# Kernel tuning notes

Hardware: AMD Instinct MI355X
Metric: run time of the kernel (lower is better)

## Reference

```python
import jax, jax.numpy as jnp
import numpy as np
from jax import lax

TAU_MIN = 0.01
TAU_MAX = 10.0
SLOW_TAU = 5.0


def setup_inputs() -> dict:
    key = jax.random.key(0)
    ks = iter(jax.random.split(key, 40))
    def p(shape, scale=0.05):
        return (jax.random.normal(next(ks), shape, jnp.float32) * scale)
    B, T, D = 1024, 512, 31
    FU, SU, H = 32, 32, 64
    inp = {
        "x": jax.random.normal(next(ks), (B, T, D), jnp.float32),
        # FlashFloodGate: Linear(62->32), Linear(32->1)
        "fg_w1": p((32, 2 * D)), "fg_b1": p((32,)),
        "fg_w2": p((1, 32)), "fg_b2": p((1,)),
        # fast LTC cell
        "fwin": p((FU, D)), "fbin": p((FU,)), "fwrec": p((FU, FU)),
        # slow LTC cell
        "swin": p((SU, D)), "sbin": p((SU,)), "swrec": p((SU, SU)),
        # fusion Linear(64->64)
        "fu_w": p((H, FU + SU)), "fu_b": p((H,)),
        # attention Linear(64->32), Linear(32->1)
        "at_w1": p((32, H)), "at_b1": p((32,)),
        "at_w2": p((1, 32)), "at_b2": p((1,)),
        # depth head Linear(64->64), Linear(64->5)
        "d_w1": p((64, H)), "d_b1": p((64,)),
        "d_w2": p((5, 64)), "d_b2": p((5,)),
        # overflow head Linear(64->64), Linear(64->32), Linear(32->1)
        "o_w1": p((64, H)), "o_b1": p((64,)),
        "o_w2": p((32, 64)), "o_b2": p((32,)),
        "o_w3": p((1, 32)), "o_b3": p((1,)),
        # intensity head Linear(64->32), Linear(32->1)
        "i_w1": p((32, H)), "i_b1": p((32,)),
        "i_w2": p((1, 32)), "i_b2": p((1,)),
    }
    return inp


def _ltc_scan(pre_tbh, w_rec, tau_tb1, h0):
    # pre_tbh: [T,B,H] precomputed W_in x + b; tau_tb1 broadcastable to [T,B,1]
    def step(h, inp):
        pre_t, tau_t = inp
        upd = jnp.tanh(pre_t + h @ w_rec.T)
        h = h + (upd - h) / tau_t
        return h, h
    _, hs = lax.scan(step, h0, (pre_tbh, tau_tb1))
    return jnp.transpose(hs, (1, 0, 2))  # [B,T,H]


def _forward(x, fg_w1, fg_b1, fg_w2, fg_b2, fwin, fbin, fwrec, swin, sbin, swrec,
             fu_w, fu_b, at_w1, at_b1, at_w2, at_b2, d_w1, d_b1, d_w2, d_b2,
             o_w1, o_b1, o_w2, o_b2, o_w3, o_b3, i_w1, i_b1, i_w2, i_b2):
    B, T, D = x.shape
    # FlashFloodGate over all timesteps (x_prev of t=0 is x_0 -> dx=0)
    dx = jnp.concatenate([jnp.zeros_like(x[:, :1]), x[:, 1:] - x[:, :-1]], axis=1)
    ci = jnp.concatenate([x, dx], axis=-1)                       # [B,T,2D]
    cs = jax.nn.sigmoid(jnp.tanh(ci @ fg_w1.T + fg_b1) @ fg_w2.T + fg_b2)  # [B,T,1]
    tau_fast = TAU_MAX - cs * (TAU_MAX - TAU_MIN)                # [B,T,1]
    # fast LTC (stepwise tau)
    pre_f = jnp.transpose(x @ fwin.T + fbin, (1, 0, 2))          # [T,B,FU]
    fast = _ltc_scan(pre_f, fwrec, jnp.transpose(tau_fast, (1, 0, 2)),
                     jnp.zeros((B, fwrec.shape[0]), x.dtype))
    # slow LTC (constant tau = 5.0, shape [B,1])
    pre_s = jnp.transpose(x @ swin.T + sbin, (1, 0, 2))          # [T,B,SU]
    slow = _ltc_scan(pre_s, swrec, jnp.full((T, 1, 1), SLOW_TAU, x.dtype),
                     jnp.zeros((B, swrec.shape[0]), x.dtype))
    # fusion
    ltc = jnp.tanh(jnp.concatenate([fast, slow], axis=-1) @ fu_w.T + fu_b)  # [B,T,H]
    # attention over time
    logits = jnp.tanh(ltc @ at_w1.T + at_b1) @ at_w2.T + at_b2   # [B,T,1]
    attn = jax.nn.softmax(logits, axis=1)
    context = jnp.sum(ltc * attn, axis=1)                        # [B,H]
    # heads (dropout is identity in eval)
    depths = jax.nn.relu(context @ d_w1.T + d_b1) @ d_w2.T + d_b2
    overflow = jax.nn.sigmoid(
        jax.nn.relu(jax.nn.relu(context @ o_w1.T + o_b1) @ o_w2.T + o_b2) @ o_w3.T + o_b3)
    intensity = jax.nn.sigmoid(jax.nn.relu(context @ i_w1.T + i_b1) @ i_w2.T + i_b2)
    return (depths, overflow, intensity)


def reference(x, fg_w1, fg_b1, fg_w2, fg_b2, fwin, fbin, fwrec, swin, sbin, swrec,
              fu_w, fu_b, at_w1, at_b1, at_w2, at_b2, d_w1, d_b1, d_w2, d_b2,
              o_w1, o_b1, o_w2, o_b2, o_w3, o_b3, i_w1, i_b1, i_w2, i_b2):
    return _forward(x, fg_w1, fg_b1, fg_w2, fg_b2, fwin, fbin, fwrec, swin, sbin,
                    swrec, fu_w, fu_b, at_w1, at_b1, at_w2, at_b2, d_w1, d_b1,
                    d_w2, d_b2, o_w1, o_b1, o_w2, o_b2, o_w3, o_b3,
                    i_w1, i_b1, i_w2, i_b2)
```

## Files before the change

kernel.cpp:

```cpp
#include <hip/hip_runtime.h>


#define T_  512
#define D_  31
#define GR_ 16
#define NG_ 32
#define NIT 36
#define L2E 1.4426950408889634f
#define TS_ 2.8853900817779268f

typedef decltype(__builtin_amdgcn_cvt_pkrtz(0.0f, 0.0f)) h2;
typedef _Float16 h8v __attribute__((ext_vector_type(8)));
typedef float    f4v __attribute__((ext_vector_type(4)));

__device__ __forceinline__ float fexp2(float x){ return __builtin_amdgcn_exp2f(x); }
__device__ __forceinline__ float frcp (float x){ return __builtin_amdgcn_rcpf(x); }
__device__ __forceinline__ float tanh_pre(float x){
    return 1.0f - 2.0f * frcp(1.0f + fexp2(x));
}
__device__ __forceinline__ h2 cvt2(float a, float b){ return __builtin_amdgcn_cvt_pkrtz(a, b); }
__device__ __forceinline__ h2 bch2(unsigned v){ return __builtin_bit_cast(h2, v); }
__device__ __forceinline__ unsigned bcu(h2 v){ return __builtin_bit_cast(unsigned, v); }

template <int CTRL>
__device__ __forceinline__ float dppf(float v){
    int r = __builtin_amdgcn_update_dpp(0, __builtin_bit_cast(int, v),
                                        CTRL, 0xf, 0xf, true);
    return __builtin_bit_cast(float, r);
}
template <int CTRL>
__device__ __forceinline__ unsigned dppu(unsigned v){
    return (unsigned)__builtin_amdgcn_update_dpp(0, (int)v, CTRL, 0xf, 0xf, true);
}
__device__ __forceinline__ unsigned swz16(unsigned v){
    return (unsigned)__builtin_amdgcn_ds_swizzle((int)v, 0x401F);
}
__device__ __forceinline__ float rsum16(float v){
    v += dppf<0xB1>(v); v += dppf<0x4E>(v); v += dppf<0x141>(v); v += dppf<0x140>(v);
    return v;
}

#if __has_builtin(__builtin_amdgcn_fdot2)
#define FDOT2(acc, a, b) (acc) = __builtin_amdgcn_fdot2((a), (b), (acc), false)
#else
#define FDOT2(acc, a, b) (acc) += (float)(a)[0]*(float)(b)[0] + (float)(a)[1]*(float)(b)[1]
#endif

#define MFMA16(A, Bf, Cf) __builtin_amdgcn_mfma_f32_16x16x32_f16((A), (Bf), (Cf), 0, 0, 0)

#define BAR() do { asm volatile("s_waitcnt lgkmcnt(0)" ::: "memory"); \
                   __builtin_amdgcn_s_barrier();                      \
                   asm volatile("" ::: "memory"); } while (0)

__launch_bounds__(256, 4)
__global__ void lnn_mf(
    const float* __restrict__ X,
    const float* __restrict__ fg_w1, const float* __restrict__ fg_b1,
    const float* __restrict__ fg_w2, const float* __restrict__ fg_b2,
    const float* __restrict__ fwin,  const float* __restrict__ fbin,
    const float* __restrict__ fwrec,
    const float* __restrict__ swin,  const float* __restrict__ sbin,
    const float* __restrict__ swrec,
    const float* __restrict__ fu_w,  const float* __restrict__ fu_b,
    const float* __restrict__ at_w1, const float* __restrict__ at_b1,
    const float* __restrict__ at_w2, const float* __restrict__ at_b2,
    const float* __restrict__ d_w1,  const float* __restrict__ d_b1,
    const float* __restrict__ d_w2,  const float* __restrict__ d_b2,
    const float* __restrict__ o_w1,  const float* __restrict__ o_b1,
    const float* __restrict__ o_w2,  const float* __restrict__ o_b2,
    const float* __restrict__ o_w3,  const float* __restrict__ o_b3,
    const float* __restrict__ i_w1,  const float* __restrict__ i_b1,
    const float* __restrict__ i_w2,  const float* __restrict__ i_b2,
    float* __restrict__ out, int B)
{
    const int b    = blockIdx.x;
    const int tx   = threadIdx.x;
    const int wid  = tx >> 6;
    const int lane = tx & 63;
    const int u    = lane & 31;
    const int hb32 = lane & 32;
    const int role = (wid + b) & 3;

    __shared__ __align__(16) float    xr_sh [4][GR_][36];
    __shared__ float    xdm   [36];
    __shared__ float    pre_sh[4][GR_][65];
    __shared__ __align__(16) float    rt_sh [4][GR_];
    __shared__ __align__(16) unsigned hpk_sh[2][GR_][36];
    __shared__ __align__(16) unsigned ltcpk [2][GR_][36];
    __shared__ __align__(16) float    pw_sh [GR_];
    __shared__ float    ctx_sh[64];

    if (tx < 64) xr_sh[tx >> 4][tx & 15][31] = 0.0f;

    if (role == 0) {
        const int col = lane & 15, kb = lane >> 4;
        h8v wB[8];
        #pragma unroll
        for (int c = 0; c < 8; ++c) {
            float wv[8];
            #pragma unroll
            for (int j = 0; j < 8; ++j) {
                const int k = kb*8 + j;
                float v = 0.0f;
                if (k < 31) {
                    const int uu = 16*(c & 1) + col;
                    if (c < 2)      v = fg_w1[uu*62 + k] + fg_w1[uu*62 + 31 + k];
                    else if (c < 4) v = fg_w1[uu*62 + 31 + k];
                    else if (c < 6) v = fwin[uu*31 + k];
                    else            v = swin[uu*31 + k];
                }
                wv[j] = v * TS_;
            }
            uint4 qq = { bcu(cvt2(wv[0],wv[1])), bcu(cvt2(wv[2],wv[3])),
                         bcu(cvt2(wv[4],wv[5])), bcu(cvt2(wv[6],wv[7])) };
            wB[c] = __builtin_bit_cast(h8v, qq);
        }
        const float b1c[2] = { fg_b1[col] * TS_, fg_b1[16 + col] * TS_ };
        const float pb[4]  = { fbin[col] * TS_, fbin[16+col] * TS_,
                               sbin[col] * TS_, sbin[16+col] * TS_ };
        const float w2n[2] = { fg_w2[col] * (-L2E), fg_w2[16+col] * (-L2E) };
        const float b2n    = fg_b2[0] * (-L2E);
        const unsigned* Xu = (const unsigned*)(X + (size_t)b * T_ * D_ + lane);
        float ypv[2] = {0.0f, 0.0f};
        asm volatile("s_waitcnt vmcnt(0)" ::: "memory");

        #pragma unroll
        for (int gg = 0; gg < 2; ++gg)
            #pragma unroll
            for (int k = 0; k < GR_; ++k)
                if (lane < 31)
                    __builtin_amdgcn_global_load_lds(
                        (const __attribute__((address_space(1))) unsigned*)(Xu + (size_t)(GR_*gg + k) * 31),
                        (__attribute__((address_space(3))) unsigned*)(&xr_sh[gg][k][0]),
                        4, 0, 0);

        for (int i = 0; i < NIT; ++i) {
            asm volatile("s_waitcnt vmcnt(16)" ::: "memory");
            BAR();
            {
                const int gq = i + 2;
                #pragma unroll
                for (int k = 0; k < GR_; ++k) {
                    int tl = GR_*gq + k; if (tl > 511) tl = 511;
                    float* dst = (gq <= NG_-1) ? &xr_sh[gq & 3][k][0] : &xdm[0];
                    if (lane < 31)
                        __builtin_amdgcn_global_load_lds(
                            (const __attribute__((address_space(1))) unsigned*)(Xu + (size_t)tl * 31),
                            (__attribute__((address_space(3))) unsigned*)dst,
                            4, 0, 0);
                }
            }
            if (i <= NG_-1) {
                const int sG = i & 3;
                const float* xrow = &xr_sh[sG][col][kb*8];
                float4 xa = *(const float4*)xrow;
                float4 xb = *(const float4*)(xrow + 4);
                uint4 aq = { bcu(cvt2(xa.x,xa.y)), bcu(cvt2(xa.z,xa.w)),
                             bcu(cvt2(xb.x,xb.y)), bcu(cvt2(xb.z,xb.w)) };
                h8v Af = __builtin_bit_cast(h8v, aq);
                f4v C[8];
                #pragma unroll
                for (int c = 0; c < 8; ++c) {
                    f4v z = {0.f, 0.f, 0.f, 0.f};
                    C[c] = MFMA16(Af, wB[c], z);
                }
                const int tb = kb * 4;
                float tp[4] = {0.f, 0.f, 0.f, 0.f};
                #pragma unroll
                for (int p = 0; p < 2; ++p) {
                    f4v G = C[p], Y = C[2+p];
                    if (i == 0) ypv[p] = __shfl(Y[0], col);
                    float ylast = __shfl(Y[3], 48 + col);
                    float yup   = __shfl(Y[3], (lane - 16) & 63);
                    float ysh0  = (kb == 0) ? ypv[p] : yup;
                    float h1v[4];
                    h1v[0] = tanh_pre(G[0] - ysh0 + b1c[p]);
                    h1v[1] = tanh_pre(G[1] - Y[0] + b1c[p]);
                    h1v[2] = tanh_pre(G[2] - Y[1] + b1c[p]);
                    h1v[3] = tanh_pre(G[3] - Y[2] + b1c[p]);
                    ypv[p] = ylast;
                    #pragma unroll
                    for (int r = 0; r < 4; ++r) tp[r] += h1v[r] * w2n[p];
                }
                float4 rtq;
                #pragma unroll
                for (int r = 0; r < 4; ++r) {
                    float s  = rsum16(tp[r]) + b2n;
                    float cs = frcp(1.0f + fexp2(s));
                    ((float*)&rtq)[r] = frcp(10.0f - 9.99f * cs);
                }
                if (col == 0) *(float4*)&rt_sh[sG][tb] = rtq;
                #pragma unroll
                for (int c = 4; c < 8; ++c) {
                    const int uo = (c < 6 ? 0 : 32) + 16*(c & 1) + col;
                    #pragma unroll
                    for (int r = 0; r < 4; ++r)
                        pre_sh[sG][tb + r][uo] = C[c][r] + pb[c-4];
                }
            }
        }
        asm volatile("s_waitcnt vmcnt(0)" ::: "memory");
    } else if (role == 1) {
        const bool slow = (lane >= 32);
        const float* W  = (slow ? swrec : fwrec) + u * 32;
        const int M0[8] = {0,2,7,5,15,13,8,10};
        const int M1[8] = {1,3,6,4,14,12,9,11};
        h2 wr[16];
        #pragma unroll
        for (int j = 0; j < 16; ++j) {
            const int x = (j & 8) ? 16 : 0;
            wr[j] = cvt2(W[u ^ M0[j & 7] ^ x] * TS_, W[u ^ M1[j & 7] ^ x] * TS_);
        }
        float h_st = 0.0f;

        for (int i = 0; i < NIT; ++i) {
            BAR();
            if (i >= 2 && i <= NG_ + 1) {
                const int gR = i - 2;
                const int sR = gR & 3;
                const int sH = gR & 1;
                float preA[GR_], rtA[GR_];
                #pragma unroll
                for (int k = 0; k < GR_; ++k)
                    preA[k] = pre_sh[sR][k][lane];
                const float4* rr = (const float4*)(&rt_sh[sR][0]);
                float4 r0 = rr[0], r1 = rr[1], r2 = rr[2], r3 = rr[3];
                {
                    float tmp[GR_] = { r0.x,r0.y,r0.z,r0.w, r1.x,r1.y,r1.z,r1.w,
                                       r2.x,r2.y,r2.z,r2.w, r3.x,r3.y,r3.z,r3.w };
                    #pragma unroll
                    for (int k = 0; k < GR_; ++k)
                        rtA[k] = slow ? 0.2f : tmp[k];
                }
                __builtin_amdgcn_s_setprio(1);
                #pragma unroll
                for (int k = 0; k < GR_; ++k) {
                    float hn = dppf<0xB1>(h_st);
                    unsigned u0 = bcu(cvt2(h_st, hn));
                    unsigned w0 = swz16(u0);
                    unsigned u1 = dppu<0x4E>(u0);
                    unsigned u2 = dppu<0x141>(u0);
                    unsigned u3 = dppu<0x141>(u1);
                    unsigned u4 = dppu<0x140>(u0);
                    unsigned u5 = dppu<0x140>(u1);
                    unsigned u6 = dppu<0x140>(u2);
                    unsigned u7 = dppu<0x140>(u3);
                    unsigned w1 = dppu<0x4E>(w0);
                    unsigned w2 = dppu<0x141>(w0);
                    unsigned w3 = dppu<0x141>(w1);
                    unsigned w4 = dppu<0x140>(w0);
                    unsigned w5 = dppu<0x140>(w1);
                    unsigned w6 = dppu<0x140>(w2);
                    unsigned w7 = dppu<0x140>(w3);
                    float a0 = 0.f, a1 = 0.f, a2 = 0.f, a3 = 0.f;
                    FDOT2(a0, bch2(u0), wr[0]);  FDOT2(a1, bch2(u1), wr[1]);
                    FDOT2(a2, bch2(u2), wr[2]);  FDOT2(a3, bch2(u3), wr[3]);
                    FDOT2(a0, bch2(u4), wr[4]);  FDOT2(a1, bch2(u5), wr[5]);
                    FDOT2(a2, bch2(u6), wr[6]);  FDOT2(a3, bch2(u7), wr[7]);
                    FDOT2(a0, bch2(w0), wr[8]);  FDOT2(a1, bch2(w1), wr[9]);
                    FDOT2(a2, bch2(w2), wr[10]); FDOT2(a3, bch2(w3), wr[11]);
                    FDOT2(a0, bch2(w4), wr[12]); FDOT2(a1, bch2(w5), wr[13]);
                    FDOT2(a2, bch2(w6), wr[14]); FDOT2(a3, bch2(w7), wr[15]);
                    float v   = (a0 + a1) + (a2 + a3);
                    float upd = tanh_pre(v + preA[k]);
                    h_st += (upd - h_st) * rtA[k];
                    float hw = dppf<0xB1>(h_st);
                    if (!(lane & 1))
                        hpk_sh[sH][k][lane >> 1] = bcu(cvt2(h_st, hw));
                }
                __builtin_amdgcn_s_setprio(0);
            }
        }
    } else if (role == 2) {
        const int col = lane & 15, kb = lane >> 4;
        h8v wF[8];
        #pragma unroll
        for (int kc = 0; kc < 2; ++kc)
            #pragma unroll
            for (int nc = 0; nc < 4; ++nc) {
                float wv[8];
                #pragma unroll
                for (int j = 0; j < 8; ++j)
                    wv[j] = fu_w[(16*nc + col)*64 + 32*kc + 8*kb + j] * TS_;
                uint4 qq = { bcu(cvt2(wv[0],wv[1])), bcu(cvt2(wv[2],wv[3])),
                             bcu(cvt2(wv[4],wv[5])), bcu(cvt2(wv[6],wv[7])) };
                wF[kc*4 + nc] = __builtin_bit_cast(h8v, qq);
            }
        const float fb4[4] = { fu_b[col] * TS_, fu_b[16+col] * TS_,
                               fu_b[32+col] * TS_, fu_b[48+col] * TS_ };

        for (int i = 0; i < NIT; ++i) {
            BAR();
            if (i >= 3 && i <= NG_ + 2) {
                const int gF = i - 3;
                const int sH = gF & 1;
                const unsigned* hrow = &hpk_sh[sH][col][0];
                uint4 a0q = *(const uint4*)(hrow + kb*4);
                uint4 a1q = *(const uint4*)(hrow + kb*4 + 16);
                h8v A0 = __builtin_bit_cast(h8v, a0q);
                h8v A1 = __builtin_bit_cast(h8v, a1q);
                const int tb = kb * 4;
                #pragma unroll
                for (int nc = 0; nc < 4; ++nc) {
                    f4v c4 = {0.f, 0.f, 0.f, 0.f};
                    c4 = MFMA16(A0, wF[nc],     c4);
                    c4 = MFMA16(A1, wF[4 + nc], c4);
                    #pragma unroll
                    for (int r = 0; r < 4; ++r) {
                        float v  = tanh_pre(c4[r] + fb4[nc]);
                        float vn = dppf<0xB1>(v);
                        h2 pk = (col & 1) ? cvt2(vn, v) : cvt2(v, vn);
                        if (!(col & 1))
                            ltcpk[gF & 1][tb + r][(16*nc + col) >> 1] = bcu(pk);
                    }
                }
            }
        }
    } else {
        const int col = lane & 15, kb = lane >> 4;
        h8v wA[4];
        #pragma unroll
        for (int kt = 0; kt < 2; ++kt)
            #pragma unroll
            for (int nt = 0; nt < 2; ++nt) {
                float wv[8];
                #pragma unroll
                for (int j = 0; j < 8; ++j)
                    wv[j] = at_w1[(nt*16 + col)*64 + kt*32 + 8*kb + j] * TS_;
                uint4 qq = { bcu(cvt2(wv[0],wv[1])), bcu(cvt2(wv[2],wv[3])),
                             bcu(cvt2(wv[4],wv[5])), bcu(cvt2(wv[6],wv[7])) };
                wA[kt*2 + nt] = __builtin_bit_cast(h8v, qq);
            }
        const float ab1v[2] = { at_b1[col] * TS_, at_b1[16 + col] * TS_ };
        const float w2L[2]  = { at_w2[col] * L2E, at_w2[16 + col] * L2E };
        const float ab2L    = at_b2[0] * L2E;
        float s_run = 0.0f, c_run = 0.0f;

        for (int i = 0; i < NIT; ++i) {
            BAR();
            if (i >= 4) {
                const int gA = i - 4;
                const int sl = gA & 1;
                const unsigned* lrow = &ltcpk[sl][col][0];
                uint4 l0q = *(const uint4*)(lrow + kb*4);
                uint4 l1q = *(const uint4*)(lrow + kb*4 + 16);
                h8v L0 = __builtin_bit_cast(h8v, l0q);
                h8v L1 = __builtin_bit_cast(h8v, l1q);
                f4v CA[2];
                #pragma unroll
                for (int nt = 0; nt < 2; ++nt) {
                    f4v c4 = {0.f, 0.f, 0.f, 0.f};
                    c4 = MFMA16(L0, wA[nt],     c4);
                    c4 = MFMA16(L1, wA[2 + nt], c4);
                    CA[nt] = c4;
                }
                float4 pwq;
                #pragma unroll
                for (int r = 0; r < 4; ++r) {
                    float s = tanh_pre(CA[0][r] + ab1v[0]) * w2L[0]
                            + tanh_pre(CA[1][r] + ab1v[1]) * w2L[1];
                    s = rsum16(s);
                    ((float*)&pwq)[r] = fexp2(s + ab2L);
                }
                if (col == 0) *(float4*)&pw_sh[kb*4] = pwq;
                const float4* pwp = (const float4*)&pw_sh[0];
                float4 q0 = pwp[0], q1 = pwp[1], q2 = pwp[2], q3 = pwp[3];
                float pwA[GR_] = { q0.x,q0.y,q0.z,q0.w, q1.x,q1.y,q1.z,q1.w,
                                   q2.x,q2.y,q2.z,q2.w, q3.x,q3.y,q3.z,q3.w };
                #pragma unroll
                for (int t = 0; t < GR_; ++t) {
                    float ltc = (float)((const _Float16*)(&ltcpk[sl][t][0]))[lane];
                    s_run += pwA[t];
                    c_run += pwA[t] * ltc;
                }
            }
        }
        ctx_sh[lane] = c_run * frcp(s_run);
    }

    __syncthreads();

    if (wid == 0) {
        float r1 = d_b1[lane];
        #pragma unroll
        for (int c = 0; c < 16; ++c) {
            float4 cq = ((const float4*)ctx_sh)[c];
            float4 wq = ((const float4*)(d_w1 + lane*64))[c];
            r1 += wq.x*cq.x + wq.y*cq.y + wq.z*cq.z + wq.w*cq.w;
        }
        r1 = fmaxf(r1, 0.0f);
        #pragma unroll
        for (int kk = 0; kk < 5; ++kk) {
            float v = d_w2[kk*64 + lane] * r1;
            v += __shfl_xor(v, 1);  v += __shfl_xor(v, 2);
            v += __shfl_xor(v, 4);  v += __shfl_xor(v, 8);
            v += __shfl_xor(v, 16); v += __shfl_xor(v, 32);
            if (lane == 0) out[b*5 + kk] = v + d_b2[kk];
        }
    } else if (wid == 1) {
        float r1 = o_b1[lane];
        #pragma unroll
        for (int c = 0; c < 16; ++c) {
            float4 cq = ((const float4*)ctx_sh)[c];
            float4 wq = ((const float4*)(o_w1 + lane*64))[c];
            r1 += wq.x*cq.x + wq.y*cq.y + wq.z*cq.z + wq.w*cq.w;
        }
        r1 = fmaxf(r1, 0.0f);
        float acc = 0.0f;
        #pragma unroll
        for (int j = 0; j < 32; ++j) {
            float rj = __shfl(r1, hb32 + j);
            acc += o_w2[u*64 + hb32 + j] * rj;
        }
        acc += __shfl_xor(acc, 32);
        float r2 = fmaxf(acc + o_b2[u], 0.0f);
        float v  = o_w3[u] * r2;
        v += __shfl_xor(v, 1);  v += __shfl_xor(v, 2);
        v += __shfl_xor(v, 4);  v += __shfl_xor(v, 8);
        v += __shfl_xor(v, 16);
        if (lane == 0) {
            float e = fexp2((v + o_b3[0]) * -L2E);
            out[5*B + b] = frcp(1.0f + e);
        }
    } else if (wid == 2) {
        float acc = 0.0f;
        #pragma unroll
        for (int c = 0; c < 8; ++c) {
            float4 cq = ((const float4*)(ctx_sh + hb32))[c];
            float4 wq = ((const float4*)(i_w1 + u*64 + hb32))[c];
            acc += wq.x*cq.x + wq.y*cq.y + wq.z*cq.z + wq.w*cq.w;
        }
        acc += __shfl_xor(acc, 32);
        float r1 = fmaxf(acc + i_b1[u], 0.0f);
        float v  = i_w2[u] * r1;
        v += __shfl_xor(v, 1);  v += __shfl_xor(v, 2);
        v += __shfl_xor(v, 4);  v += __shfl_xor(v, 8);
        v += __shfl_xor(v, 16);
        if (lane == 0) {
            float e = fexp2((v + i_b2[0]) * -L2E);
            out[6*B + b] = frcp(1.0f + e);
        }
    }
}

extern "C" void kernel_launch(void* const* d_in, const int* in_sizes, int n_in,
                              void* d_out, int out_size, void* d_ws, size_t ws_size,
                              hipStream_t stream) {
    (void)n_in; (void)out_size; (void)d_ws; (void)ws_size;
    const float* X     = (const float*)d_in[0];
    const float* fg_w1 = (const float*)d_in[1];
    const float* fg_b1 = (const float*)d_in[2];
    const float* fg_w2 = (const float*)d_in[3];
    const float* fg_b2 = (const float*)d_in[4];
    const float* fwin  = (const float*)d_in[5];
    const float* fbin  = (const float*)d_in[6];
    const float* fwrec = (const float*)d_in[7];
    const float* swin  = (const float*)d_in[8];
    const float* sbin  = (const float*)d_in[9];
    const float* swrec = (const float*)d_in[10];
    const float* fu_w  = (const float*)d_in[11];
    const float* fu_b  = (const float*)d_in[12];
    const float* at_w1 = (const float*)d_in[13];
    const float* at_b1 = (const float*)d_in[14];
    const float* at_w2 = (const float*)d_in[15];
    const float* at_b2 = (const float*)d_in[16];
    const float* d_w1  = (const float*)d_in[17];
    const float* d_b1  = (const float*)d_in[18];
    const float* d_w2  = (const float*)d_in[19];
    const float* d_b2  = (const float*)d_in[20];
    const float* o_w1  = (const float*)d_in[21];
    const float* o_b1  = (const float*)d_in[22];
    const float* o_w2  = (const float*)d_in[23];
    const float* o_b2  = (const float*)d_in[24];
    const float* o_w3  = (const float*)d_in[25];
    const float* o_b3  = (const float*)d_in[26];
    const float* i_w1  = (const float*)d_in[27];
    const float* i_b1  = (const float*)d_in[28];
    const float* i_w2  = (const float*)d_in[29];
    const float* i_b2  = (const float*)d_in[30];
    float* out = (float*)d_out;

    const int B = in_sizes[0] / (T_ * D_);
    dim3 grid(B), block(256);
    hipLaunchKernelGGL(lnn_mf, grid, block, 0, stream,
        X, fg_w1, fg_b1, fg_w2, fg_b2, fwin, fbin, fwrec, swin, sbin, swrec,
        fu_w, fu_b, at_w1, at_b1, at_w2, at_b2, d_w1, d_b1, d_w2, d_b2,
        o_w1, o_b1, o_w2, o_b2, o_w3, o_b3, i_w1, i_b1, i_w2, i_b2, out, B);
}
```

Baseline: 94.41 us.

## Load x tiles with contiguous 16-byte LDS DMA and drop store predicates

```diff
diff --git a/kernel.cpp b/kernel.cpp
--- a/kernel.cpp
+++ b/kernel.cpp
@@ -81,8 +81,7 @@
     const int hb32 = lane & 32;
     const int role = (wid + b) & 3;
 
-    __shared__ __align__(16) float    xr_sh [4][GR_][36];
-    __shared__ float    xdm   [36];
+    __shared__ __align__(16) float    xfl   [4][512];
     __shared__ float    pre_sh[4][GR_][65];
     __shared__ __align__(16) float    rt_sh [4][GR_];
     __shared__ __align__(16) unsigned hpk_sh[2][GR_][36];
@@ -90,7 +89,7 @@
     __shared__ __align__(16) float    pw_sh [GR_];
     __shared__ float    ctx_sh[64];
 
-    if (tx < 64) xr_sh[tx >> 4][tx & 15][31] = 0.0f;
+    if (tx < 64) xfl[tx >> 4][496 + (tx & 15)] = 0.0f;
 
     if (role == 0) {
         const int col = lane & 15, kb = lane >> 4;
@@ -120,43 +119,48 @@
                                sbin[col] * TS_, sbin[16+col] * TS_ };
         const float w2n[2] = { fg_w2[col] * (-L2E), fg_w2[16+col] * (-L2E) };
         const float b2n    = fg_b2[0] * (-L2E);
-        const unsigned* Xu = (const unsigned*)(X + (size_t)b * T_ * D_ + lane);
+        const unsigned* Xg = (const unsigned*)(X + (size_t)b * T_ * D_);
         float ypv[2] = {0.0f, 0.0f};
         asm volatile("s_waitcnt vmcnt(0)" ::: "memory");
 
         #pragma unroll
-        for (int gg = 0; gg < 2; ++gg)
-            #pragma unroll
-            for (int k = 0; k < GR_; ++k)
-                if (lane < 31)
+        for (int gg = 0; gg < 2; ++gg) {
+            const unsigned* src = Xg + (size_t)gg * 496;
+            __builtin_amdgcn_global_load_lds(
+                (const __attribute__((address_space(1))) unsigned*)(src + lane*4),
+                (__attribute__((address_space(3))) unsigned*)(&xfl[gg][0]),
+                16, 0, 0);
+            if (lane < 60)
+                __builtin_amdgcn_global_load_lds(
+                    (const __attribute__((address_space(1))) unsigned*)(src + 256 + lane*4),
+                    (__attribute__((address_space(3))) unsigned*)(&xfl[gg][256]),
+                    16, 0, 0);
+        }
+
+        for (int i = 0; i < NIT; ++i) {
+            if (i < 31) { asm volatile("s_waitcnt vmcnt(2)" ::: "memory"); }
+            else        { asm volatile("s_waitcnt vmcnt(0)" ::: "memory"); }
+            BAR();
+            if (i < 30) {
+                const int gq = i + 2;
+                const unsigned* src = Xg + (size_t)gq * 496;
+                __builtin_amdgcn_global_load_lds(
+                    (const __attribute__((address_space(1))) unsigned*)(src + lane*4),
+                    (__attribute__((address_space(3))) unsigned*)(&xfl[gq & 3][0]),
+                    16, 0, 0);
+                if (lane < 60)
                     __builtin_amdgcn_global_load_lds(
-                        (const __attribute__((address_space(1))) unsigned*)(Xu + (size_t)(GR_*gg + k) * 31),
-                        (__attribute__((address_space(3))) unsigned*)(&xr_sh[gg][k][0]),
-                        4, 0, 0);
-
-        for (int i = 0; i < NIT; ++i) {
-            asm volatile("s_waitcnt vmcnt(16)" ::: "memory");
-            BAR();
-            {
-                const int gq = i + 2;
-                #pragma unroll
-                for (int k = 0; k < GR_; ++k) {
-                    int tl = GR_*gq + k; if (tl > 511) tl = 511;
-                    float* dst = (gq <= NG_-1) ? &xr_sh[gq & 3][k][0] : &xdm[0];
-                    if (lane < 31)
-                        __builtin_amdgcn_global_load_lds(
-                            (const __attribute__((address_space(1))) unsigned*)(Xu + (size_t)tl * 31),
-                            (__attribute__((address_space(3))) unsigned*)dst,
-                            4, 0, 0);
-                }
+                        (const __attribute__((address_space(1))) unsigned*)(src + 256 + lane*4),
+                        (__attribute__((address_space(3))) unsigned*)(&xfl[gq & 3][256]),
+                        16, 0, 0);
             }
             if (i <= NG_-1) {
                 const int sG = i & 3;
-                const float* xrow = &xr_sh[sG][col][kb*8];
-                float4 xa = *(const float4*)xrow;
-                float4 xb = *(const float4*)(xrow + 4);
-                uint4 aq = { bcu(cvt2(xa.x,xa.y)), bcu(cvt2(xa.z,xa.w)),
-                             bcu(cvt2(xb.x,xb.y)), bcu(cvt2(xb.z,xb.w)) };
+                const float* xr = &xfl[sG][col*31 + kb*8];
+                float x0 = xr[0], x1 = xr[1], x2 = xr[2], x3 = xr[3];
+                float x4 = xr[4], x5 = xr[5], x6 = xr[6], x7 = xr[7];
+                uint4 aq = { bcu(cvt2(x0,x1)), bcu(cvt2(x2,x3)),
+                             bcu(cvt2(x4,x5)), bcu(cvt2(x6,x7)) };
                 h8v Af = __builtin_bit_cast(h8v, aq);
                 f4v C[8];
                 #pragma unroll
@@ -265,8 +269,8 @@
                     float upd = tanh_pre(v + preA[k]);
                     h_st += (upd - h_st) * rtA[k];
                     float hw = dppf<0xB1>(h_st);
-                    if (!(lane & 1))
-                        hpk_sh[sH][k][lane >> 1] = bcu(cvt2(h_st, hw));
+                    h2 pk = (lane & 1) ? cvt2(hw, h_st) : cvt2(h_st, hw);
+                    hpk_sh[sH][k][lane >> 1] = bcu(pk);
                 }
                 __builtin_amdgcn_s_setprio(0);
             }
@@ -310,8 +314,7 @@
                         float v  = tanh_pre(c4[r] + fb4[nc]);
                         float vn = dppf<0xB1>(v);
                         h2 pk = (col & 1) ? cvt2(vn, v) : cvt2(v, vn);
-                        if (!(col & 1))
-                            ltcpk[gF & 1][tb + r][(16*nc + col) >> 1] = bcu(pk);
+                        ltcpk[gF & 1][tb + r][(16*nc + col) >> 1] = bcu(pk);
                     }
                 }
             }
```

New measurement: 106.2 us. 12.5% more time.
